# Optimization experiments

Hardware: AMD Instinct MI355X
Metric: run time of the kernel (lower is better)

The kernel has to match this reference:

```python
import jax, jax.numpy as jnp
import numpy as np

N, E, F_IN, EDGE_DIM, H, C, NUM_RELS = 20000, 160000, 64, 8, 4, 128, 4


def setup_inputs() -> dict:
    key = jax.random.key(0)
    ks = jax.random.split(key, 20)
    def rn(k, shape, s=0.05):
        return jax.random.normal(k, shape, jnp.float32) * s
    return {
        "x": rn(ks[0], (N, F_IN), 1.0),
        "edge_index": jax.random.randint(ks[1], (2, E), 0, N, dtype=jnp.int32),
        "edge_features": rn(ks[2], (E, EDGE_DIM), 1.0),
        "W1": rn(ks[3], (F_IN, H * C)), "a_src1": rn(ks[4], (H, C)), "a_dst1": rn(ks[5], (H, C)),
        "We1": rn(ks[6], (EDGE_DIM, H * C)), "a_e1": rn(ks[7], (H, C)), "b1": jnp.zeros((H * C,), jnp.float32),
        "W2": rn(ks[8], (H * C, H * C)), "a_src2": rn(ks[9], (H, C)), "a_dst2": rn(ks[10], (H, C)),
        "We2": rn(ks[11], (EDGE_DIM, H * C)), "a_e2": rn(ks[12], (H, C)), "b2": jnp.zeros((H * C,), jnp.float32),
        "Wd1": rn(ks[13], (2 * H * C, 256)), "bd1": jnp.zeros((256,), jnp.float32),
        "Wd2": rn(ks[14], (256, NUM_RELS)), "bd2": jnp.zeros((NUM_RELS,), jnp.float32),
    }


def _add_self_loops(ei, ea, n):
    # PyG add_self_loops with fill_value='mean': self-loop edge_attr is the
    # mean of incoming edge_attr per destination node (0 if no incoming edges).
    dst = ei[1]
    s = jax.ops.segment_sum(ea, dst, num_segments=n)
    cnt = jax.ops.segment_sum(jnp.ones((ea.shape[0], 1), ea.dtype), dst, num_segments=n)
    mean = s / jnp.maximum(cnt, 1.0)
    loop = jnp.arange(n, dtype=ei.dtype)
    ei2 = jnp.concatenate([ei, jnp.stack([loop, loop])], axis=1)
    ea2 = jnp.concatenate([ea, mean], axis=0)
    return ei2, ea2


def _gat_conv(x, ei, ea, W, a_s, a_d, We, a_e, b, n):
    ei, ea = _add_self_loops(ei, ea, n)
    src, dst = ei[0], ei[1]
    xp = (x @ W).reshape(n, H, C)                      # [N,H,C]
    alpha_s = jnp.einsum('nhc,hc->nh', xp, a_s)        # [N,H]
    alpha_d = jnp.einsum('nhc,hc->nh', xp, a_d)        # [N,H]
    ep = (ea @ We).reshape(-1, H, C)                   # [E',H,C]
    alpha_e = jnp.einsum('ehc,hc->eh', ep, a_e)        # [E',H]
    alpha = alpha_s[src] + alpha_d[dst] + alpha_e
    alpha = jax.nn.leaky_relu(alpha, 0.2)
    # segment softmax over edges sharing a destination node
    m = jax.ops.segment_max(alpha, dst, num_segments=n)
    ex = jnp.exp(alpha - m[dst])
    den = jax.ops.segment_sum(ex, dst, num_segments=n)
    w = ex / den[dst]                                   # [E',H]
    out = jax.ops.segment_sum(xp[src] * w[..., None], dst, num_segments=n)  # [N,H,C]
    return out.reshape(n, H * C) + b


def reference(x, edge_index, edge_features, W1, a_src1, a_dst1, We1, a_e1, b1,
              W2, a_src2, a_dst2, We2, a_e2, b2, Wd1, bd1, Wd2, bd2):
    n = x.shape[0]
    z = jax.nn.elu(_gat_conv(x, edge_index, edge_features, W1, a_src1, a_dst1, We1, a_e1, b1, n))
    z = jax.nn.elu(_gat_conv(z, edge_index, edge_features, W2, a_src2, a_dst2, We2, a_e2, b2, n))
    src, dst = edge_index[0], edge_index[1]
    rel = jnp.concatenate([z[src], z[dst]], axis=1)     # [E, 2*512]
    h = rel @ Wd1 + bd1                                 # dropout is identity at inference
    return jax.nn.sigmoid(h @ Wd2 + bd2)
```

## Files before the change

### kernel.cpp

```cpp
#include <hip/hip_runtime.h>
#include <hip/hip_bf16.h>
#include <math.h>

#define N_NODES 20000
#define N_EDGES 160000
#define FIN 64
#define EDGE_DIM 8
#define H_HEADS 4
#define C_CH 128
#define HC 512
#define NUM_RELS 4
#define E_TOT (N_EDGES + N_NODES)
#define E_PAD 320256

typedef __bf16 bf16x8 __attribute__((ext_vector_type(8)));
typedef float f32x4 __attribute__((ext_vector_type(4)));
typedef unsigned short u16x8 __attribute__((ext_vector_type(8)));

#define NZ4 ((N_NODES + E_PAD) / 4)
#define NM4 (E_PAD / 4)
__global__ void k_fill(int4* __restrict__ zbase, int4* __restrict__ mbase) {
    int tid = blockIdx.x * 256 + threadIdx.x;
    if (tid < NZ4) {
        zbase[tid] = make_int4(0, 0, 0, 0);
    } else if (tid < NZ4 + NM4) {
        mbase[tid - NZ4] = make_int4(-1, -1, -1, -1);
    }
}

#define NX4 (N_NODES * FIN / 4)
#define W1T (HC * FIN)
#define W2T (HC * HC)
#define NCVTB ((NX4 + W1T + W2T) / 256)
__global__ void k_prep_all(const float* __restrict__ x, __bf16* __restrict__ xb,
                           const float* __restrict__ W1, __bf16* __restrict__ Wt1,
                           const float* __restrict__ W2, __bf16* __restrict__ Wt2,
                           const float* __restrict__ We1, const float* __restrict__ ae1,
                           const float* __restrict__ We2, const float* __restrict__ ae2,
                           float* __restrict__ q1, float* __restrict__ q2,
                           const float* __restrict__ Wd1, const float* __restrict__ Wd2,
                           const float* __restrict__ bd1, const float* __restrict__ bd2,
                           float* __restrict__ M, float* __restrict__ cvec,
                           const float* __restrict__ as1, const float* __restrict__ ad1,
                           float* __restrict__ w1as, float* __restrict__ w1ad) {
    int bid = blockIdx.x;
    if (bid < NCVTB) {
        int tid = bid * 256 + threadIdx.x;
        if (tid < NX4) {
            float4 v = *(const float4*)(x + (size_t)tid * 4);
            __bf16 o[4] = {(__bf16)v.x, (__bf16)v.y, (__bf16)v.z, (__bf16)v.w};
            *(ushort2*)(xb + (size_t)tid * 4) = *(ushort2*)o;
            *(ushort2*)(xb + (size_t)tid * 4 + 2) = *(ushort2*)(o + 2);
        } else if (tid < NX4 + W1T) {
            int t = tid - NX4;
            int n = t / FIN, k = t % FIN;
            Wt1[n * FIN + k] = (__bf16)W1[(size_t)k * HC + n];
        } else {
            int t = tid - NX4 - W1T;
            int n = t >> 9, k = t & 511;
            Wt2[n * HC + k] = (__bf16)W2[(size_t)k * HC + n];
        }
        return;
    }
    int pb = bid - NCVTB;
    if (pb == 16) {
        int t = threadIdx.x;
        if (t >= 64) return;
        const float* We = (t < 32) ? We1 : We2;
        const float* ae = (t < 32) ? ae1 : ae2;
        float* q = (t < 32) ? q1 : q2;
        int i = t & 31, h = i >> 3, d = i & 7;
        float s = 0.f;
        for (int c = 0; c < 128; ++c) s += We[d * 512 + h * 128 + c] * ae[h * 128 + c];
        q[i] = s;
    } else if (pb == 17 || pb == 18) {
        int t = threadIdx.x;
        int h = t >> 6, k = t & 63;
        const float* av = (pb == 17) ? as1 : ad1;
        float* outp = (pb == 17) ? w1as : w1ad;
        float s = 0.f;
        for (int c = 0; c < 128; ++c) s += W1[(size_t)k * HC + h * 128 + c] * av[h * 128 + c];
        outp[h * 64 + k] = s;
    } else {
        int tid = pb * 256 + threadIdx.x;
        int i = tid >> 2, r = tid & 3;
        float s = 0.f;
        for (int k = 0; k < 256; ++k) s += Wd1[i * 256 + k] * Wd2[k * 4 + r];
        M[tid] = s;
        if (tid < 4) {
            float c = 0.f;
            for (int k = 0; k < 256; ++k) c += bd1[k] * Wd2[k * 4 + tid];
            cvec[tid] = c + bd2[tid];
        }
    }
}

#define LDP 40
__global__ __launch_bounds__(256)
void k_gemm_bf16(const __bf16* __restrict__ A, const __bf16* __restrict__ Bt,
                 __bf16* __restrict__ Ch, int M, int K) {
    __shared__ __bf16 As[128 * LDP];
    __shared__ __bf16 Bs[128 * LDP];

    int nwg = gridDim.x;
    int f = blockIdx.x;
    int q = nwg >> 3, r = nwg & 7;
    int xcd = f & 7, idx = f >> 3;
    int wg = (xcd < r ? xcd * (q + 1) : r * (q + 1) + (xcd - r) * q) + idx;
    int by = wg >> 2, bx = wg & 3;
    int br = by * 128, bc = bx * 128;

    const int t = threadIdx.x;
    const int lane = t & 63;
    const int wid = t >> 6;
    const int wr = wid >> 1, wc = wid & 1;
    const int l15 = lane & 15, lkg = lane >> 4;

    const int srow = t >> 1, shalf = (t & 1) * 16;
    const int agr = br + srow;
    const __bf16* Ap = A + (size_t)agr * K + shalf;
    const __bf16* Bp = Bt + (size_t)(bc + srow) * K + shalf;

    f32x4 acc[4][4] = {};

    for (int k0 = 0; k0 < K; k0 += 32) {
        u16x8 av0 = {}, av1 = {};
        if (agr < M) {
            av0 = *(const u16x8*)(Ap + k0);
            av1 = *(const u16x8*)(Ap + k0 + 8);
        }
        u16x8 bv0 = *(const u16x8*)(Bp + k0);
        u16x8 bv1 = *(const u16x8*)(Bp + k0 + 8);
        *(u16x8*)(As + srow * LDP + shalf) = av0;
        *(u16x8*)(As + srow * LDP + shalf + 8) = av1;
        *(u16x8*)(Bs + srow * LDP + shalf) = bv0;
        *(u16x8*)(Bs + srow * LDP + shalf + 8) = bv1;
        __syncthreads();

        bf16x8 a[4], b[4];
        #pragma unroll
        for (int m = 0; m < 4; ++m)
            a[m] = *(const bf16x8*)(As + (wr * 64 + m * 16 + l15) * LDP + lkg * 8);
        #pragma unroll
        for (int n = 0; n < 4; ++n)
            b[n] = *(const bf16x8*)(Bs + (wc * 64 + n * 16 + l15) * LDP + lkg * 8);
        #pragma unroll
        for (int m = 0; m < 4; ++m)
            #pragma unroll
            for (int n = 0; n < 4; ++n)
                acc[m][n] = __builtin_amdgcn_mfma_f32_16x16x32_bf16(a[m], b[n], acc[m][n], 0, 0, 0);
        __syncthreads();
    }

    #pragma unroll
    for (int m = 0; m < 4; ++m) {
        int rbase = br + wr * 64 + m * 16 + lkg * 4;
        #pragma unroll
        for (int n = 0; n < 4; ++n) {
            int lcol = wc * 64 + n * 16 + l15;
            #pragma unroll
            for (int rg = 0; rg < 4; ++rg) {
                int gr = rbase + rg;
                if (gr < M)
                    Ch[((size_t)bx * N_NODES + gr) * 128 + lcol] = (__bf16)acc[m][n][rg];
            }
        }
    }
}

__global__ __launch_bounds__(256)
void k_gemm_head(const __bf16* __restrict__ aggb, const __bf16* __restrict__ Wt1,
                 const float* __restrict__ b1, __bf16* __restrict__ z1b, int M) {
    __shared__ __bf16 As[128 * LDP];
    __shared__ __bf16 Bs[128 * LDP];
    const int h = blockIdx.x;
    const int br = blockIdx.y * 128;

    const int t = threadIdx.x;
    const int lane = t & 63;
    const int wid = t >> 6;
    const int wr = wid >> 1, wc = wid & 1;
    const int l15 = lane & 15, lkg = lane >> 4;

    const int srow = t >> 1, shalf = (t & 1) * 16;
    const int agr = br + srow;
    const __bf16* Ap = aggb + (size_t)agr * 256 + h * 64 + shalf;
    const __bf16* Bp = Wt1 + (size_t)(h * 128 + srow) * 64 + shalf;

    f32x4 acc[4][4] = {};

    #pragma unroll
    for (int k0 = 0; k0 < 64; k0 += 32) {
        u16x8 av0 = {}, av1 = {};
        if (agr < M) {
            av0 = *(const u16x8*)(Ap + k0);
            av1 = *(const u16x8*)(Ap + k0 + 8);
        }
        u16x8 bv0 = *(const u16x8*)(Bp + k0);
        u16x8 bv1 = *(const u16x8*)(Bp + k0 + 8);
        *(u16x8*)(As + srow * LDP + shalf) = av0;
        *(u16x8*)(As + srow * LDP + shalf + 8) = av1;
        *(u16x8*)(Bs + srow * LDP + shalf) = bv0;
        *(u16x8*)(Bs + srow * LDP + shalf + 8) = bv1;
        __syncthreads();

        bf16x8 a[4], b[4];
        #pragma unroll
        for (int m = 0; m < 4; ++m)
            a[m] = *(const bf16x8*)(As + (wr * 64 + m * 16 + l15) * LDP + lkg * 8);
        #pragma unroll
        for (int n = 0; n < 4; ++n)
            b[n] = *(const bf16x8*)(Bs + (wc * 64 + n * 16 + l15) * LDP + lkg * 8);
        #pragma unroll
        for (int m = 0; m < 4; ++m)
            #pragma unroll
            for (int n = 0; n < 4; ++n)
                acc[m][n] = __builtin_amdgcn_mfma_f32_16x16x32_bf16(a[m], b[n], acc[m][n], 0, 0, 0);
        __syncthreads();
    }

    #pragma unroll
    for (int m = 0; m < 4; ++m) {
        int rbase = br + wr * 64 + m * 16 + lkg * 4;
        #pragma unroll
        for (int n = 0; n < 4; ++n) {
            int gcol = h * 128 + wc * 64 + n * 16 + l15;
            float bias = b1[gcol];
            #pragma unroll
            for (int rg = 0; rg < 4; ++rg) {
                int gr = rbase + rg;
                if (gr < M) {
                    float v = acc[m][n][rg] + bias;
                    v = (v > 0.f) ? v : expm1f(v);
                    z1b[(size_t)gr * HC + gcol] = (__bf16)v;
                }
            }
        }
    }
}

__global__ void k_count(const int* __restrict__ ei, int* __restrict__ counts) {
    int e = blockIdx.x * 256 + threadIdx.x;
    if (e >= E_TOT) return;
    int dst = (e < N_EDGES) ? ei[N_EDGES + e] : (e - N_EDGES);
    atomicAdd(counts + dst, 1);
}

__global__ __launch_bounds__(1024)
void k_scan(const int* __restrict__ counts, int* __restrict__ row_start,
            int* __restrict__ nxt) {
    __shared__ int part[1024];
    int t = threadIdx.x;
    int base = t * 20;
    int pre[20];
    int s = 0;
    #pragma unroll
    for (int i = 0; i < 20; ++i) {
        int idx = base + i;
        int c = (idx < N_NODES) ? ((counts[idx] + 7) & ~7) : 0;
        pre[i] = s; s += c;
    }
    part[t] = s;
    __syncthreads();
    for (int off = 1; off < 1024; off <<= 1) {
        int v = (t >= off) ? part[t - off] : 0;
        __syncthreads();
        part[t] += v;
        __syncthreads();
    }
    int excl = (t == 0) ? 0 : part[t - 1];
    #pragma unroll
    for (int i = 0; i < 20; ++i) {
        int idx = base + i;
        if (idx < N_NODES) { int v = excl + pre[i]; row_start[idx] = v; nxt[idx] = v; }
    }
    if (t == 1023) row_start[N_NODES] = part[1023];
}

__global__ void k_scatter(const int* __restrict__ ei, int* __restrict__ nxt,
                          int* __restrict__ csr_src, int* __restrict__ csr_eid,
                          int* __restrict__ csr_dst) {
    int e = blockIdx.x * 256 + threadIdx.x;
    if (e >= E_TOT) return;
    int src, dst;
    if (e < N_EDGES) { src = ei[e]; dst = ei[N_EDGES + e]; }
    else             { src = dst = e - N_EDGES; }
    int pos = atomicAdd(nxt + dst, 1);
    csr_src[pos] = src;
    csr_eid[pos] = e;
    csr_dst[pos] = dst;
}

__global__ void k_mean_csr(const int* __restrict__ row_start, const int* __restrict__ csr_eid,
                           const float* __restrict__ ef, float* __restrict__ meanf) {
    int n = blockIdx.x * 32 + (threadIdx.x >> 3);
    int d = threadIdx.x & 7;
    if (n >= N_NODES) return;
    int rs = row_start[n], re = row_start[n + 1];
    float s = 0.f; int c = 0;
    for (int i = rs; i < re; ++i) {
        unsigned eid = (unsigned)csr_eid[i];
        if (eid < N_EDGES) { s += ef[(size_t)eid * 8 + d]; ++c; }
    }
    meanf[n * 8 + d] = s / fmaxf((float)c, 1.f);
}

__global__ __launch_bounds__(256)
void k_nodeab(const __bf16* __restrict__ xb, const float* __restrict__ w1as,
              const float* __restrict__ w1ad, float* __restrict__ as_,
              float* __restrict__ ad_) {
    int n = blockIdx.x * 4 + (threadIdx.x >> 6);
    int lane = threadIdx.x & 63;
    if (n >= N_NODES) return;
    float xv = (float)xb[(size_t)n * 64 + lane];
    float s[4], d[4];
    #pragma unroll
    for (int h = 0; h < 4; ++h) {
        s[h] = xv * w1as[h * 64 + lane];
        d[h] = xv * w1ad[h * 64 + lane];
    }
    #pragma unroll
    for (int off = 32; off; off >>= 1) {
        #pragma unroll
        for (int h = 0; h < 4; ++h) {
            s[h] += __shfl_xor(s[h], off);
            d[h] += __shfl_xor(d[h], off);
        }
    }
    if (lane == 0) {
        *(float4*)(as_ + n * 4) = make_float4(s[0], s[1], s[2], s[3]);
        *(float4*)(ad_ + n * 4) = make_float4(d[0], d[1], d[2], d[3]);
    }
}

__global__ __launch_bounds__(256)
void k_node_alpha_hm(const __bf16* __restrict__ xph, const float* __restrict__ a_s,
                     const float* __restrict__ a_d, float* __restrict__ as_,
                     float* __restrict__ ad_) {
    int n = blockIdx.x * 4 + (threadIdx.x >> 6);
    int lane = threadIdx.x & 63;
    if (n >= N_NODES) return;
    float s[4], d[4];
    #pragma unroll
    for (int h = 0; h < 4; ++h) {
        ushort2 xv = *(const ushort2*)(xph + ((size_t)h * N_NODES + n) * 128 + lane * 2);
        __bf16 b0 = *(const __bf16*)&xv.x, b1v = *(const __bf16*)&xv.y;
        float x0 = (float)b0, x1 = (float)b1v;
        s[h] = x0 * a_s[h * 128 + lane * 2] + x1 * a_s[h * 128 + lane * 2 + 1];
        d[h] = x0 * a_d[h * 128 + lane * 2] + x1 * a_d[h * 128 + lane * 2 + 1];
    }
    #pragma unroll
    for (int off = 32; off; off >>= 1) {
        #pragma unroll
        for (int h = 0; h < 4; ++h) {
            s[h] += __shfl_xor(s[h], off);
            d[h] += __shfl_xor(d[h], off);
        }
    }
    if (lane == 0) {
        *(float4*)(as_ + n * 4) = make_float4(s[0], s[1], s[2], s[3]);
        *(float4*)(ad_ + n * 4) = make_float4(d[0], d[1], d[2], d[3]);
    }
}

__global__ void k_edge_ex(const int* __restrict__ csr_src, const int* __restrict__ csr_dst,
                          const int* __restrict__ csr_eid, const float* __restrict__ ef,
                          const float* __restrict__ meanf, const float* __restrict__ q,
                          const float* __restrict__ as_, const float* __restrict__ ad_,
                          float* __restrict__ wbuf) {
    int i = blockIdx.x * 256 + threadIdx.x;
    if (i >= E_PAD) return;
    int eid = csr_eid[i];
    if (eid == -1) {
        *(float4*)(wbuf + (size_t)i * 4) = make_float4(0.f, 0.f, 0.f, 0.f);
        return;
    }
    int src = csr_src[i], dst = csr_dst[i];
    const float* fe = (eid < N_EDGES) ? (ef + (size_t)eid * 8)
                                      : (meanf + (size_t)(eid - N_EDGES) * 8);
    float f[8];
    #pragma unroll
    for (int d = 0; d < 8; ++d) f[d] = fe[d];
    float4 asv = *(const float4*)(as_ + src * 4);
    float4 adv = *(const float4*)(ad_ + dst * 4);
    const float* asp = &asv.x;
    const float* adp = &adv.x;
    float4 o;
    float* op = &o.x;
    #pragma unroll
    for (int h = 0; h < 4; ++h) {
        float ae = 0.f;
        #pragma unroll
        for (int d = 0; d < 8; ++d) ae += f[d] * q[h * 8 + d];
        float a = asp[h] + adp[h] + ae;
        a = (a > 0.f) ? a : 0.2f * a;
        op[h] = expf(a);
    }
    *(float4*)(wbuf + (size_t)i * 4) = o;
}

__global__ __launch_bounds__(256)
void k_gather1(const int* __restrict__ row_start, const int* __restrict__ csr_src,
               const float* __restrict__ wbuf, const __bf16* __restrict__ xb,
               __bf16* __restrict__ aggb) {
    int wv = threadIdx.x >> 6;
    int n = blockIdx.x * 4 + wv;
    int lane = threadIdx.x & 63;
    if (n >= N_NODES) return;
    int rs = row_start[n], re = row_start[n + 1];
    float acc[4] = {};
    float den[4] = {};

    for (int i = rs; i < re; i += 8) {
        unsigned short xr[8];
        float4 wr[8];
        #pragma unroll
        for (int p = 0; p < 8; ++p) {
            int sp = csr_src[i + p];
            xr[p] = *(const unsigned short*)(xb + (size_t)sp * 64 + lane);
            wr[p] = *(const float4*)(wbuf + (size_t)(i + p) * 4);
        }
        __builtin_amdgcn_sched_barrier(0);
        #pragma unroll
        for (int p = 0; p < 8; ++p) {
            float xv = (float)*(const __bf16*)&xr[p];
            acc[0] += wr[p].x * xv; den[0] += wr[p].x;
            acc[1] += wr[p].y * xv; den[1] += wr[p].y;
            acc[2] += wr[p].z * xv; den[2] += wr[p].z;
            acc[3] += wr[p].w * xv; den[3] += wr[p].w;
        }
    }
    #pragma unroll
    for (int h = 0; h < 4; ++h)
        aggb[(size_t)n * 256 + h * 64 + lane] = (__bf16)(acc[h] / den[h]);
}

__global__ __launch_bounds__(256)
void k_gather2h(const int* __restrict__ row_start, const int* __restrict__ csr_src,
                const float* __restrict__ wbuf, const __bf16* __restrict__ xph,
                const float* __restrict__ b2, __bf16* __restrict__ zh) {
    int h = blockIdx.y;
    int wv = threadIdx.x >> 6;
    int n = blockIdx.x * 4 + wv;
    int lane = threadIdx.x & 63;
    if (n >= N_NODES) return;
    int rs = row_start[n], re = row_start[n + 1];
    const __bf16* xbase = xph + (size_t)h * N_NODES * 128 + lane * 2;
    float a0 = 0.f, a1 = 0.f, den = 0.f;

    for (int i = rs; i < re; i += 8) {
        unsigned xr[8];
        float wr[8];
        #pragma unroll
        for (int p = 0; p < 8; ++p) {
            int sp = csr_src[i + p];
            wr[p] = wbuf[(size_t)(i + p) * 4 + h];
            xr[p] = *(const unsigned*)(xbase + (size_t)sp * 128);
        }
        __builtin_amdgcn_sched_barrier(0);
        #pragma unroll
        for (int p = 0; p < 8; ++p) {
            __bf16 b0 = *(const __bf16*)&xr[p];
            __bf16 b1v = *((const __bf16*)&xr[p] + 1);
            den += wr[p];
            a0 += wr[p] * (float)b0;
            a1 += wr[p] * (float)b1v;
        }
    }
    float inv = 1.f / den;
    float v0 = a0 * inv + b2[h * 128 + lane * 2];
    float v1 = a1 * inv + b2[h * 128 + lane * 2 + 1];
    v0 = (v0 > 0.f) ? v0 : expm1f(v0);
    v1 = (v1 > 0.f) ? v1 : expm1f(v1);
    __bf16 o[2] = {(__bf16)v0, (__bf16)v1};
    *(ushort*)(zh + ((size_t)h * N_NODES + n) * 128 + lane * 2) = *(ushort*)&o[0];
    *(ushort*)(zh + ((size_t)h * N_NODES + n) * 128 + lane * 2 + 1) = *(ushort*)&o[1];
}

__global__ __launch_bounds__(256)
void k_uv(const __bf16* __restrict__ zh, const float* __restrict__ Mm,
          float* __restrict__ U, float* __restrict__ V) {
    int n = blockIdx.x * 4 + (threadIdx.x >> 6);
    int lane = threadIdx.x & 63;
    if (n >= N_NODES) return;
    int h = lane >> 4;
    bf16x8 zv = *(const bf16x8*)(zh + ((size_t)h * N_NODES + n) * 128 + (lane & 15) * 8);
    float u[4] = {}, v[4] = {};
    #pragma unroll
    for (int k = 0; k < 8; ++k) {
        float z = (float)zv[k];
        int fidx = lane * 8 + k;
        #pragma unroll
        for (int r = 0; r < 4; ++r) {
            u[r] += z * Mm[fidx * 4 + r];
            v[r] += z * Mm[(512 + fidx) * 4 + r];
        }
    }
    #pragma unroll
    for (int r = 0; r < 4; ++r) {
        #pragma unroll
        for (int off = 32; off; off >>= 1) {
            u[r] += __shfl_xor(u[r], off);
            v[r] += __shfl_xor(v[r], off);
        }
    }
    if (lane == 0) {
        *(float4*)(U + n * 4) = make_float4(u[0], u[1], u[2], u[3]);
        *(float4*)(V + n * 4) = make_float4(v[0], v[1], v[2], v[3]);
    }
}

__global__ void k_edge_out(const int* __restrict__ ei, const float* __restrict__ U,
                           const float* __restrict__ V, const float* __restrict__ cvec,
                           float* __restrict__ out) {
    int e = blockIdx.x * 256 + threadIdx.x;
    if (e >= N_EDGES) return;
    float4 u = *(const float4*)(U + (size_t)ei[e] * 4);
    float4 v = *(const float4*)(V + (size_t)ei[N_EDGES + e] * 4);
    float4 c = *(const float4*)cvec;
    float4 o;
    o.x = 1.f / (1.f + expf(-(u.x + v.x + c.x)));
    o.y = 1.f / (1.f + expf(-(u.y + v.y + c.y)));
    o.z = 1.f / (1.f + expf(-(u.z + v.z + c.z)));
    o.w = 1.f / (1.f + expf(-(u.w + v.w + c.w)));
    *(float4*)(out + (size_t)e * 4) = o;
}

extern "C" void kernel_launch(void* const* d_in, const int* in_sizes, int n_in,
                              void* d_out, int out_size, void* d_ws, size_t ws_size,
                              hipStream_t stream) {
    (void)in_sizes; (void)n_in; (void)out_size; (void)ws_size;
    const float* x      = (const float*)d_in[0];
    const int*   ei     = (const int*)d_in[1];
    const float* ef     = (const float*)d_in[2];
    const float* W1     = (const float*)d_in[3];
    const float* a_src1 = (const float*)d_in[4];
    const float* a_dst1 = (const float*)d_in[5];
    const float* We1    = (const float*)d_in[6];
    const float* a_e1   = (const float*)d_in[7];
    const float* b1     = (const float*)d_in[8];
    const float* W2     = (const float*)d_in[9];
    const float* a_src2 = (const float*)d_in[10];
    const float* a_dst2 = (const float*)d_in[11];
    const float* We2    = (const float*)d_in[12];
    const float* a_e2   = (const float*)d_in[13];
    const float* b2     = (const float*)d_in[14];
    const float* Wd1    = (const float*)d_in[15];
    const float* bd1    = (const float*)d_in[16];
    const float* Wd2    = (const float*)d_in[17];
    const float* bd2    = (const float*)d_in[18];
    float* out = (float*)d_out;

    float* wbuf   = (float*)d_ws;
    float* as_    = wbuf + (size_t)E_PAD * 4;
    float* ad_    = as_ + N_NODES * 4;
    float* meanf  = ad_ + N_NODES * 4;
    float* q1     = meanf + N_NODES * 8;
    float* q2     = q1 + 32;
    float* w1as   = q2 + 32;
    float* w1ad   = w1as + 256;
    float* Mm     = w1ad + 256;
    float* cv     = Mm + 4096;
    float* U      = cv + 4;
    float* V      = U + N_NODES * 4;
    int* row_start = (int*)(V + N_NODES * 4);
    int* nxt       = row_start + 20004;
    int* counts    = nxt + N_NODES;
    int* csr_src   = counts + N_NODES;
    int* csr_eid   = csr_src + E_PAD;
    int* csr_dst   = csr_eid + E_PAD;
    __bf16* xb   = (__bf16*)(csr_dst + E_PAD);
    __bf16* aggb = xb + (size_t)N_NODES * FIN;
    __bf16* z1b  = aggb + (size_t)N_NODES * 256;
    __bf16* xph2 = z1b + (size_t)N_NODES * HC;
    __bf16* Wt1  = xph2 + (size_t)N_NODES * HC;
    __bf16* Wt2  = Wt1 + HC * FIN;
    __bf16* zh   = z1b;

    k_fill<<<(NZ4 + NM4 + 255) / 256, 256, 0, stream>>>((int4*)counts, (int4*)csr_eid);
    k_count<<<(E_TOT + 255) / 256, 256, 0, stream>>>(ei, counts);
    k_scan<<<1, 1024, 0, stream>>>(counts, row_start, nxt);
    k_scatter<<<(E_TOT + 255) / 256, 256, 0, stream>>>(ei, nxt, csr_src, csr_eid, csr_dst);
    k_mean_csr<<<(N_NODES + 31) / 32, 256, 0, stream>>>(row_start, csr_eid, ef, meanf);
    k_prep_all<<<NCVTB + 19, 256, 0, stream>>>(x, xb, W1, Wt1, W2, Wt2,
                                               We1, a_e1, We2, a_e2, q1, q2,
                                               Wd1, Wd2, bd1, bd2, Mm, cv,
                                               a_src1, a_dst1, w1as, w1ad);

    const int nblk = (N_NODES + 3) / 4;
    const int nby = (N_NODES + 127) / 128;

    k_nodeab<<<nblk, 256, 0, stream>>>(xb, w1as, w1ad, as_, ad_);
    k_edge_ex<<<(E_PAD + 255) / 256, 256, 0, stream>>>(csr_src, csr_dst, csr_eid, ef, meanf,
                                                       q1, as_, ad_, wbuf);
    k_gather1<<<nblk, 256, 0, stream>>>(row_start, csr_src, wbuf, xb, aggb);
    k_gemm_head<<<dim3(4, nby), 256, 0, stream>>>(aggb, Wt1, b1, z1b, N_NODES);

    k_gemm_bf16<<<nby * 4, 256, 0, stream>>>(z1b, Wt2, xph2, N_NODES, HC);
    k_node_alpha_hm<<<nblk, 256, 0, stream>>>(xph2, a_src2, a_dst2, as_, ad_);
    k_edge_ex<<<(E_PAD + 255) / 256, 256, 0, stream>>>(csr_src, csr_dst, csr_eid, ef, meanf,
                                                       q2, as_, ad_, wbuf);
    k_gather2h<<<dim3(nblk, 4), 256, 0, stream>>>(row_start, csr_src, wbuf, xph2, b2, zh);
    k_uv<<<nblk, 256, 0, stream>>>(zh, Mm, U, V);

    k_edge_out<<<(N_EDGES + 255) / 256, 256, 0, stream>>>(ei, U, V, cv, out);
}
```

Before: 265.9 us.

## Split gather wavefronts into four edge groups with vector loads and shuffle reduction

The two aggregation kernels now split each 64-lane wavefront into four 16-lane groups. Each group handles a different edge and loads 4 or 8 bf16 channels per lane as one vector, and the groups are combined with cross-lane shuffles at the end. Because of this, CSR row padding drops from a multiple of 8 to a multiple of 4, which shrinks the padded edge buffer. The aim is more independent loads in flight per wavefront, wider memory accesses and fewer padded dummy edges. The cost is extra shuffle-reduction work and more registers per thread.

```diff
diff --git a/kernel.cpp b/kernel.cpp
--- a/kernel.cpp
+++ b/kernel.cpp
@@ -11,9 +11,10 @@
 #define HC 512
 #define NUM_RELS 4
 #define E_TOT (N_EDGES + N_NODES)
-#define E_PAD 320256
+#define E_PAD 240000
 
 typedef __bf16 bf16x8 __attribute__((ext_vector_type(8)));
+typedef __bf16 bf16x4 __attribute__((ext_vector_type(4)));
 typedef float f32x4 __attribute__((ext_vector_type(4)));
 typedef unsigned short u16x8 __attribute__((ext_vector_type(8)));
 
@@ -257,7 +258,7 @@
     #pragma unroll
     for (int i = 0; i < 20; ++i) {
         int idx = base + i;
-        int c = (idx < N_NODES) ? ((counts[idx] + 7) & ~7) : 0;
+        int c = (idx < N_NODES) ? ((counts[idx] + 3) & ~3) : 0;
         pre[i] = s; s += c;
     }
     part[t] = s;
@@ -407,32 +408,47 @@
     int n = blockIdx.x * 4 + wv;
     int lane = threadIdx.x & 63;
     if (n >= N_NODES) return;
+    int p = lane >> 4;
+    int cg = lane & 15;
     int rs = row_start[n], re = row_start[n + 1];
-    float acc[4] = {};
+    float acc[4][4] = {};
     float den[4] = {};
 
-    for (int i = rs; i < re; i += 8) {
-        unsigned short xr[8];
-        float4 wr[8];
-        #pragma unroll
-        for (int p = 0; p < 8; ++p) {
-            int sp = csr_src[i + p];
-            xr[p] = *(const unsigned short*)(xb + (size_t)sp * 64 + lane);
-            wr[p] = *(const float4*)(wbuf + (size_t)(i + p) * 4);
-        }
-        __builtin_amdgcn_sched_barrier(0);
-        #pragma unroll
-        for (int p = 0; p < 8; ++p) {
-            float xv = (float)*(const __bf16*)&xr[p];
-            acc[0] += wr[p].x * xv; den[0] += wr[p].x;
-            acc[1] += wr[p].y * xv; den[1] += wr[p].y;
-            acc[2] += wr[p].z * xv; den[2] += wr[p].z;
-            acc[3] += wr[p].w * xv; den[3] += wr[p].w;
-        }
-    }
-    #pragma unroll
-    for (int h = 0; h < 4; ++h)
-        aggb[(size_t)n * 256 + h * 64 + lane] = (__bf16)(acc[h] / den[h]);
+    for (int i = rs + p; i < re; i += 4) {
+        int sp = csr_src[i];
+        float4 w4 = *(const float4*)(wbuf + (size_t)i * 4);
+        bf16x4 xv = *(const bf16x4*)(xb + (size_t)sp * 64 + cg * 4);
+        float xf[4];
+        #pragma unroll
+        for (int k = 0; k < 4; ++k) xf[k] = (float)xv[k];
+        den[0] += w4.x; den[1] += w4.y; den[2] += w4.z; den[3] += w4.w;
+        #pragma unroll
+        for (int k = 0; k < 4; ++k) {
+            acc[0][k] += w4.x * xf[k];
+            acc[1][k] += w4.y * xf[k];
+            acc[2][k] += w4.z * xf[k];
+            acc[3][k] += w4.w * xf[k];
+        }
+    }
+    #pragma unroll
+    for (int off = 16; off <= 32; off <<= 1) {
+        #pragma unroll
+        for (int h = 0; h < 4; ++h) {
+            den[h] += __shfl_xor(den[h], off);
+            #pragma unroll
+            for (int k = 0; k < 4; ++k) acc[h][k] += __shfl_xor(acc[h][k], off);
+        }
+    }
+    if (p == 0) {
+        #pragma unroll
+        for (int h = 0; h < 4; ++h) {
+            float inv = 1.f / den[h];
+            bf16x4 o;
+            #pragma unroll
+            for (int k = 0; k < 4; ++k) o[k] = (__bf16)(acc[h][k] * inv);
+            *(bf16x4*)(aggb + (size_t)n * 256 + h * 64 + cg * 4) = o;
+        }
+    }
 }
 
 __global__ __launch_bounds__(256)
@@ -444,37 +460,37 @@
     int n = blockIdx.x * 4 + wv;
     int lane = threadIdx.x & 63;
     if (n >= N_NODES) return;
+    int p = lane >> 4;
+    int cg = lane & 15;
     int rs = row_start[n], re = row_start[n + 1];
-    const __bf16* xbase = xph + (size_t)h * N_NODES * 128 + lane * 2;
-    float a0 = 0.f, a1 = 0.f, den = 0.f;
-
-    for (int i = rs; i < re; i += 8) {
-        unsigned xr[8];
-        float wr[8];
-        #pragma unroll
-        for (int p = 0; p < 8; ++p) {
-            int sp = csr_src[i + p];
-            wr[p] = wbuf[(size_t)(i + p) * 4 + h];
-            xr[p] = *(const unsigned*)(xbase + (size_t)sp * 128);
-        }
-        __builtin_amdgcn_sched_barrier(0);
-        #pragma unroll
-        for (int p = 0; p < 8; ++p) {
-            __bf16 b0 = *(const __bf16*)&xr[p];
-            __bf16 b1v = *((const __bf16*)&xr[p] + 1);
-            den += wr[p];
-            a0 += wr[p] * (float)b0;
-            a1 += wr[p] * (float)b1v;
-        }
-    }
-    float inv = 1.f / den;
-    float v0 = a0 * inv + b2[h * 128 + lane * 2];
-    float v1 = a1 * inv + b2[h * 128 + lane * 2 + 1];
-    v0 = (v0 > 0.f) ? v0 : expm1f(v0);
-    v1 = (v1 > 0.f) ? v1 : expm1f(v1);
-    __bf16 o[2] = {(__bf16)v0, (__bf16)v1};
-    *(ushort*)(zh + ((size_t)h * N_NODES + n) * 128 + lane * 2) = *(ushort*)&o[0];
-    *(ushort*)(zh + ((size_t)h * N_NODES + n) * 128 + lane * 2 + 1) = *(ushort*)&o[1];
+    const __bf16* xbase = xph + (size_t)h * N_NODES * 128 + cg * 8;
+    float acc[8] = {};
+    float den = 0.f;
+
+    for (int i = rs + p; i < re; i += 4) {
+        int sp = csr_src[i];
+        float w = wbuf[(size_t)i * 4 + h];
+        bf16x8 xv = *(const bf16x8*)(xbase + (size_t)sp * 128);
+        den += w;
+        #pragma unroll
+        for (int k = 0; k < 8; ++k) acc[k] += w * (float)xv[k];
+    }
+    #pragma unroll
+    for (int off = 16; off <= 32; off <<= 1) {
+        den += __shfl_xor(den, off);
+        #pragma unroll
+        for (int k = 0; k < 8; ++k) acc[k] += __shfl_xor(acc[k], off);
+    }
+    if (p == 0) {
+        float inv = 1.f / den;
+        bf16x8 o;
+        #pragma unroll
+        for (int k = 0; k < 8; ++k) {
+            float v = acc[k] * inv + b2[h * 128 + cg * 8 + k];
+            o[k] = (__bf16)((v > 0.f) ? v : expm1f(v));
+        }
+        *(bf16x8*)(zh + ((size_t)h * N_NODES + n) * 128 + cg * 8) = o;
+    }
 }
 
 __global__ __launch_bounds__(256)
```

Measured after the change: 288.0 us. 8.3% more time.
